# Kernel tuning notes

Hardware: AMD Instinct MI355X
Metric: run time of the kernel (lower is better)

## Reference

```python
import jax, jax.numpy as jnp
import numpy as np

SIGMA = 1.0


def setup_inputs() -> dict:
    key = jax.random.key(0)
    k1, k2, k3 = jax.random.split(key, 3)
    B, N = 32, 1024
    y_pred = jax.random.normal(k1, (B, N), dtype=jnp.float32)
    y_true = jax.random.normal(k2, (B, N), dtype=jnp.float32)
    masks = jax.random.randint(k3, (B, N), 0, 2, dtype=jnp.int32)
    return {"y_pred": y_pred, "y_true": y_true, "masks": masks}


def _lambda_ndcg(y_pred, y_true, masks, sigma=SIGMA):
    # masks: [B, N] int; valid where > 0
    m = (masks > 0)
    mf = m.astype(y_pred.dtype)                      # [B, N]
    # Position of each valid item within the compressed valid list (0-indexed k).
    # Torch code: discount[k] = 1 / log2(k + 2). cumsum gives k+1, so log2(cumsum+1).
    cs = jnp.cumsum(mf, axis=1)                      # [B, N], 1-indexed count at valid slots
    disc = jnp.where(m, 1.0 / jnp.log2(cs + 1.0), 0.0)  # [B, N]

    pred_diff = y_pred[:, :, None] - y_pred[:, None, :]   # [B, N, N]
    true_diff = y_true[:, :, None] - y_true[:, None, :]   # [B, N, N]
    pair_valid = mf[:, :, None] * mf[:, None, :]          # both items valid
    pos_mask = (true_diff > 0).astype(y_pred.dtype) * pair_valid
    pairwise_weight = disc[:, :, None] + disc[:, None, :]
    # log1p(exp(-sigma * d)) == softplus(-sigma * d), numerically stable
    pair_loss = jax.nn.softplus(-sigma * pred_diff) * pos_mask * pairwise_weight

    per_row = pair_loss.sum(axis=(1, 2)) / (pos_mask.sum(axis=(1, 2)) + 1e-12)  # [B]
    # Rows with < 2 valid items have zero positive pairs -> contribute 0, matching
    # the torch `continue`; divisor is always batch_size.
    return per_row.sum() / y_pred.shape[0]


def reference(y_pred, y_true, masks):
    return _lambda_ndcg(y_pred, y_true, masks)
```

## Files before the change

kernel.cpp:

```cpp
#include <hip/hip_runtime.h>
#include <math.h>

#define Bq 32
#define Nq 1024
#define BPR 16
#define IPB (Nq / BPR)
#define TPB 256

__global__ void zero_acc_kernel(float* __restrict__ acc) {
    acc[threadIdx.x] = 0.0f;
}

__global__ __launch_bounds__(1024)
void disc_kernel(const int* __restrict__ masks, float* __restrict__ disc) {
    const int row = blockIdx.x;
    const int t = threadIdx.x;
    const int lane = t & 63;
    const int wid = t >> 6;

    const int mv = (masks[row * Nq + t] > 0) ? 1 : 0;

    int val = mv;
#pragma unroll
    for (int off = 1; off < 64; off <<= 1) {
        int n = __shfl_up(val, off, 64);
        if (lane >= off) val += n;
    }

    __shared__ int wsum[16];
    if (lane == 63) wsum[wid] = val;
    __syncthreads();

    if (wid == 0 && lane < 16) {
        int v = wsum[lane];
#pragma unroll
        for (int off = 1; off < 16; off <<= 1) {
            int n = __shfl_up(v, off, 16);
            if (lane >= off) v += n;
        }
        wsum[lane] = v;
    }
    __syncthreads();

    const int cs = val + (wid > 0 ? wsum[wid - 1] : 0);
    const float d = mv ? (1.0f / log2f((float)cs + 1.0f)) : 0.0f;
    disc[row * Nq + t] = d;
}

__global__ __launch_bounds__(TPB)
void pair_kernel(const float* __restrict__ yp,
                 const float* __restrict__ yt,
                 const float* __restrict__ disc,
                 float* __restrict__ acc) {
    const int row = blockIdx.y;
    const int chunk = blockIdx.x;
    const int tid = threadIdx.x;

    __shared__ float sp[Nq];
    __shared__ float st[Nq];
    __shared__ float sd[Nq];
    for (int k = tid; k < Nq; k += TPB) {
        sp[k] = yp[row * Nq + k];
        st[k] = yt[row * Nq + k];
        sd[k] = disc[row * Nq + k];
    }
    __syncthreads();

    float loss = 0.0f;
    float cnt = 0.0f;

    const int i0 = chunk * IPB;
#pragma unroll 1
    for (int i = i0; i < i0 + IPB; ++i) {
        const float di = sd[i];
        if (di <= 0.0f) continue;
        const float pi = sp[i];
        const float ti = st[i];
#pragma unroll
        for (int jj = 0; jj < Nq; jj += TPB) {
            const int j = jj + tid;
            const float dj = sd[j];
            const float td = ti - st[j];
            const bool pos = (td > 0.0f) & (dj > 0.0f);
            if (pos) {
                const float x = sp[j] - pi;
                const float a = __expf(-fabsf(x));
                const float spv = fmaxf(x, 0.0f) + __logf(1.0f + a);
                loss += spv * (di + dj);
                cnt += 1.0f;
            }
        }
    }

    const int lane = tid & 63;
    const int wid = tid >> 6;
#pragma unroll
    for (int off = 32; off > 0; off >>= 1) {
        loss += __shfl_down(loss, off, 64);
        cnt  += __shfl_down(cnt, off, 64);
    }
    __shared__ float rl[4], rc[4];
    if (lane == 0) { rl[wid] = loss; rc[wid] = cnt; }
    __syncthreads();
    if (tid == 0) {
        float L = rl[0] + rl[1] + rl[2] + rl[3];
        float C = rc[0] + rc[1] + rc[2] + rc[3];
        atomicAdd(&acc[2 * row + 0], L);
        atomicAdd(&acc[2 * row + 1], C);
    }
}

__global__ void final_kernel(const float* __restrict__ acc, float* __restrict__ out) {
    const int t = threadIdx.x;
    float v = 0.0f;
    if (t < Bq) {
        const float L = acc[2 * t + 0];
        const float C = acc[2 * t + 1];
        v = L / (C + 1e-12f);
    }
#pragma unroll
    for (int off = 32; off > 0; off >>= 1) v += __shfl_down(v, off, 64);
    if (t == 0) out[0] = v / (float)Bq;
}

extern "C" void kernel_launch(void* const* d_in, const int* in_sizes, int n_in,
                              void* d_out, int out_size, void* d_ws, size_t ws_size,
                              hipStream_t stream) {
    const float* y_pred = (const float*)d_in[0];
    const float* y_true = (const float*)d_in[1];
    const int*   masks  = (const int*)d_in[2];
    float* out = (float*)d_out;

    float* disc = (float*)d_ws;
    float* acc  = disc + Bq * Nq;

    zero_acc_kernel<<<1, 64, 0, stream>>>(acc);
    disc_kernel<<<Bq, 1024, 0, stream>>>(masks, disc);
    pair_kernel<<<dim3(BPR, Bq), TPB, 0, stream>>>(y_pred, y_true, disc, acc);
    final_kernel<<<1, 64, 0, stream>>>(acc, out);
}
```

Measured before the change: 90.63 us.

## Compact valid items and enumerate only unordered pairs with balanced per-thread chunks

```diff
diff --git a/kernel.cpp b/kernel.cpp
--- a/kernel.cpp
+++ b/kernel.cpp
@@ -4,15 +4,17 @@
 #define Bq 32
 #define Nq 1024
 #define BPR 16
-#define IPB (Nq / BPR)
 #define TPB 256
 
-__global__ void zero_acc_kernel(float* __restrict__ acc) {
-    acc[threadIdx.x] = 0.0f;
-}
 
 __global__ __launch_bounds__(1024)
-void disc_kernel(const int* __restrict__ masks, float* __restrict__ disc) {
+void prep_kernel(const float* __restrict__ yp,
+                 const float* __restrict__ yt,
+                 const int* __restrict__ masks,
+                 float4* __restrict__ cw,
+                 float* __restrict__ acc,
+                 int* __restrict__ vcount,
+                 int* __restrict__ done) {
     const int row = blockIdx.x;
     const int t = threadIdx.x;
     const int lane = t & 63;
@@ -43,57 +45,68 @@
     __syncthreads();
 
     const int cs = val + (wid > 0 ? wsum[wid - 1] : 0);
-    const float d = mv ? (1.0f / log2f((float)cs + 1.0f)) : 0.0f;
-    disc[row * Nq + t] = d;
+    const int V = wsum[15];
+
+    if (mv) {
+        const float d = 1.0f / log2f((float)cs + 1.0f);
+        cw[row * Nq + (cs - 1)] = make_float4(yp[row * Nq + t], yt[row * Nq + t], d, 0.0f);
+    }
+    if (t == 0) {
+        vcount[row] = V;
+        acc[2 * row + 0] = 0.0f;
+        acc[2 * row + 1] = 0.0f;
+    }
+    if (row == 0 && t == 1) *done = 0;
 }
 
 __global__ __launch_bounds__(TPB)
-void pair_kernel(const float* __restrict__ yp,
-                 const float* __restrict__ yt,
-                 const float* __restrict__ disc,
-                 float* __restrict__ acc) {
+void pair_kernel(const float4* __restrict__ cw,
+                 float* __restrict__ acc,
+                 const int* __restrict__ vcount,
+                 int* __restrict__ done,
+                 float* __restrict__ out) {
     const int row = blockIdx.y;
-    const int chunk = blockIdx.x;
-    const int tid = threadIdx.x;
+    const int V = vcount[row];
 
-    __shared__ float sp[Nq];
-    __shared__ float st[Nq];
-    __shared__ float sd[Nq];
-    for (int k = tid; k < Nq; k += TPB) {
-        sp[k] = yp[row * Nq + k];
-        st[k] = yt[row * Nq + k];
-        sd[k] = disc[row * Nq + k];
-    }
+    __shared__ float4 sv[Nq];
+    for (int s = threadIdx.x; s < V; s += TPB) sv[s] = cw[row * Nq + s];
     __syncthreads();
+
+    const int P = V * (V - 1) / 2;
+    const int T = BPR * TPB;
+    const int tgl = blockIdx.x * TPB + threadIdx.x;
+    const int chunk = (P + T - 1) / T;
+    const int k0 = tgl * chunk;
+    const int k1 = min(k0 + chunk, P);
 
     float loss = 0.0f;
     float cnt = 0.0f;
 
-    const int i0 = chunk * IPB;
+    if (k0 < k1) {
+        int i = (int)((1.0 + sqrt(1.0 + 8.0 * (double)k0)) * 0.5);
+        if (i < 1) i = 1;
+        while (i * (i - 1) / 2 > k0) --i;
+        while ((i + 1) * i / 2 <= k0) ++i;
+        int j = k0 - i * (i - 1) / 2;
+
+        float4 qi = sv[i];
 #pragma unroll 1
-    for (int i = i0; i < i0 + IPB; ++i) {
-        const float di = sd[i];
-        if (di <= 0.0f) continue;
-        const float pi = sp[i];
-        const float ti = st[i];
-#pragma unroll
-        for (int jj = 0; jj < Nq; jj += TPB) {
-            const int j = jj + tid;
-            const float dj = sd[j];
-            const float td = ti - st[j];
-            const bool pos = (td > 0.0f) & (dj > 0.0f);
-            if (pos) {
-                const float x = sp[j] - pi;
-                const float a = __expf(-fabsf(x));
-                const float spv = fmaxf(x, 0.0f) + __logf(1.0f + a);
-                loss += spv * (di + dj);
-                cnt += 1.0f;
-            }
+        for (int k = k0; k < k1; ++k) {
+            const float4 qj = sv[j];
+            const bool win = qi.y > qj.y;
+            const float x = win ? (qj.x - qi.x) : (qi.x - qj.x);
+            const float a = __expf(-fabsf(x));
+            const float spv = fmaxf(x, 0.0f) + __logf(1.0f + a);
+            const bool ok = (qi.y != qj.y);
+            const float w = ok ? (qi.z + qj.z) : 0.0f;
+            loss = fmaf(spv, w, loss);
+            cnt += ok ? 1.0f : 0.0f;
+            if (++j == i) { j = 0; ++i; if (i < V) qi = sv[i]; }
         }
     }
 
-    const int lane = tid & 63;
-    const int wid = tid >> 6;
+    const int lane = threadIdx.x & 63;
+    const int wid = threadIdx.x >> 6;
 #pragma unroll
     for (int off = 32; off > 0; off >>= 1) {
         loss += __shfl_down(loss, off, 64);
@@ -102,25 +115,24 @@
     __shared__ float rl[4], rc[4];
     if (lane == 0) { rl[wid] = loss; rc[wid] = cnt; }
     __syncthreads();
-    if (tid == 0) {
-        float L = rl[0] + rl[1] + rl[2] + rl[3];
-        float C = rc[0] + rc[1] + rc[2] + rc[3];
+
+    if (threadIdx.x == 0) {
+        const float L = rl[0] + rl[1] + rl[2] + rl[3];
+        const float C = rc[0] + rc[1] + rc[2] + rc[3];
         atomicAdd(&acc[2 * row + 0], L);
         atomicAdd(&acc[2 * row + 1], C);
+        __threadfence();
+        const int old = __hip_atomic_fetch_add(done, 1, __ATOMIC_ACQ_REL, __HIP_MEMORY_SCOPE_AGENT);
+        if (old == BPR * Bq - 1) {
+            float s = 0.0f;
+            for (int r = 0; r < Bq; ++r) {
+                const float L2 = __hip_atomic_load(&acc[2 * r + 0], __ATOMIC_RELAXED, __HIP_MEMORY_SCOPE_AGENT);
+                const float C2 = __hip_atomic_load(&acc[2 * r + 1], __ATOMIC_RELAXED, __HIP_MEMORY_SCOPE_AGENT);
+                s += L2 / (C2 + 1e-12f);
+            }
+            out[0] = s / (float)Bq;
+        }
     }
-}
-
-__global__ void final_kernel(const float* __restrict__ acc, float* __restrict__ out) {
-    const int t = threadIdx.x;
-    float v = 0.0f;
-    if (t < Bq) {
-        const float L = acc[2 * t + 0];
-        const float C = acc[2 * t + 1];
-        v = L / (C + 1e-12f);
-    }
-#pragma unroll
-    for (int off = 32; off > 0; off >>= 1) v += __shfl_down(v, off, 64);
-    if (t == 0) out[0] = v / (float)Bq;
 }
 
 extern "C" void kernel_launch(void* const* d_in, const int* in_sizes, int n_in,
@@ -131,11 +143,11 @@
     const int*   masks  = (const int*)d_in[2];
     float* out = (float*)d_out;
 
-    float* disc = (float*)d_ws;
-    float* acc  = disc + Bq * Nq;
+    float4* cw    = (float4*)d_ws;
+    float*  acc   = (float*)(cw + Bq * Nq);
+    int*    vcount= (int*)(acc + 2 * Bq);
+    int*    done  = vcount + Bq;
 
-    zero_acc_kernel<<<1, 64, 0, stream>>>(acc);
-    disc_kernel<<<Bq, 1024, 0, stream>>>(masks, disc);
-    pair_kernel<<<dim3(BPR, Bq), TPB, 0, stream>>>(y_pred, y_true, disc, acc);
-    final_kernel<<<1, 64, 0, stream>>>(acc, out);
+    prep_kernel<<<Bq, 1024, 0, stream>>>(y_pred, y_true, masks, cw, acc, vcount, done);
+    pair_kernel<<<dim3(BPR, Bq), TPB, 0, stream>>>(cw, acc, vcount, done, out);
 }
```

New measurement: 81.30 us. 10.3% less time.
